# Kernel tuning notes

Measured on AMD Instinct MI355X. Metric: run time of the kernel, lower is better.

The kernel has to match this reference:

```python
import jax, jax.numpy as jnp
import numpy as np


def setup_inputs() -> dict:
    key = jax.random.key(0)
    k1, k2 = jax.random.split(key)
    B, S, V = 4, 2048, 32000
    y_pred = jax.random.normal(k1, (B, S, V), dtype=jnp.float32)
    y_true = jax.random.randint(k2, (B, S), 0, V, dtype=jnp.int64)
    return {"y_pred": y_pred, "y_true": y_true, "pad_id": 0}


def reference(y_pred, y_true, pad_id):
    # Shift: predict token t+1 from position t (per the torch loop's [:-1]/[1:]).
    logits = y_pred[:, :-1, :]        # (B, S-1, V)
    targets = y_true[:, 1:]           # (B, S-1)
    logp = jax.nn.log_softmax(logits, axis=-1)
    # Gather log-prob of the true token: fused log-softmax + gather.
    nll = -jnp.take_along_axis(logp, targets[..., None], axis=-1)[..., 0]  # (B, S-1)
    mask = (targets != pad_id).astype(logits.dtype)
    # Per-sequence mean over non-pad tokens, then mean over batch.
    per_seq = jnp.sum(nll * mask, axis=-1) / jnp.sum(mask, axis=-1)        # (B,)
    return jnp.mean(per_seq)
```

## Files before the change

kernel.cpp:

```cpp
#include <hip/hip_runtime.h>
#include <math.h>

#define VOCAB 32000
#define SEQ   2048
#define SM1   2047
#define BATCH 4

__global__ __launch_bounds__(256)
void ce_row_kernel(const float* __restrict__ y_pred,
                   const int*   __restrict__ y_true,
                   const int*   __restrict__ pad_id_p,
                   float* __restrict__ row_nll,
                   float* __restrict__ row_msk) {
    const int row = blockIdx.x;
    const int b   = row / SM1;
    const int s   = row % SM1;
    const int tid = threadIdx.x;

    const float*  rowp  = y_pred + ((size_t)b * SEQ + s) * (size_t)VOCAB;
    const float4* rowp4 = (const float4*)rowp;

    float m    = -INFINITY;
    float ssum = 0.0f;
    for (int i = tid; i < VOCAB / 4; i += 256) {
        float4 v  = rowp4[i];
        float  m4 = fmaxf(fmaxf(v.x, v.y), fmaxf(v.z, v.w));
        if (m4 > m) {
            ssum *= __expf(m - m4);
            m = m4;
        }
        ssum += __expf(v.x - m) + __expf(v.y - m)
              + __expf(v.z - m) + __expf(v.w - m);
    }

    __shared__ float sm_m[256];
    __shared__ float sm_s[256];
    sm_m[tid] = m;
    sm_s[tid] = ssum;
    __syncthreads();
    for (int off = 128; off > 0; off >>= 1) {
        if (tid < off) {
            float m1 = sm_m[tid],       s1 = sm_s[tid];
            float m2 = sm_m[tid + off], s2 = sm_s[tid + off];
            float mm = fmaxf(m1, m2);
            sm_m[tid] = mm;
            sm_s[tid] = s1 * __expf(m1 - mm) + s2 * __expf(m2 - mm);
        }
        __syncthreads();
    }

    if (tid == 0) {
        const int tgt = y_true[b * SEQ + s + 1];
        const int pad = pad_id_p[0];
        const float xt  = rowp[tgt];
        const float nll = logf(sm_s[0]) + sm_m[0] - xt;
        const float mk  = (tgt != pad) ? 1.0f : 0.0f;
        row_nll[row] = nll * mk;
        row_msk[row] = mk;
    }
}

__global__ __launch_bounds__(256)
void ce_final_kernel(const float* __restrict__ row_nll,
                     const float* __restrict__ row_msk,
                     float* __restrict__ out) {
    __shared__ float sm[256];
    const int tid = threadIdx.x;
    float acc = 0.0f;
    for (int b = 0; b < BATCH; ++b) {
        float sn = 0.0f, sc = 0.0f;
        for (int i = tid; i < SM1; i += 256) {
            sn += row_nll[b * SM1 + i];
            sc += row_msk[b * SM1 + i];
        }
        sm[tid] = sn; __syncthreads();
        for (int off = 128; off > 0; off >>= 1) {
            if (tid < off) sm[tid] += sm[tid + off];
            __syncthreads();
        }
        float tot_n = sm[0];
        __syncthreads();
        sm[tid] = sc; __syncthreads();
        for (int off = 128; off > 0; off >>= 1) {
            if (tid < off) sm[tid] += sm[tid + off];
            __syncthreads();
        }
        float tot_c = sm[0];
        __syncthreads();
        acc += tot_n / tot_c;
    }
    if (tid == 0) out[0] = acc / (float)BATCH;
}

extern "C" void kernel_launch(void* const* d_in, const int* in_sizes, int n_in,
                              void* d_out, int out_size, void* d_ws, size_t ws_size,
                              hipStream_t stream) {
    const float* y_pred = (const float*)d_in[0];
    const int*   y_true = (const int*)d_in[1];
    const int*   pad_id = (const int*)d_in[2];
    float* out = (float*)d_out;

    float* row_nll = (float*)d_ws;
    float* row_msk = row_nll + BATCH * SM1;

    ce_row_kernel<<<BATCH * SM1, 256, 0, stream>>>(y_pred, y_true, pad_id,
                                                   row_nll, row_msk);
    ce_final_kernel<<<1, 256, 0, stream>>>(row_nll, row_msk, out);
}
```

Before: 198.6 us.

## Use 320-thread exact-trip loop, nontemporal loads, and wave-shuffle online-softmax reduction

The row kernel now runs 320 threads so the 8000 float4 chunks divide exactly into 25 iterations, unrolled by 5. Loads use nontemporal hints, the sum is split into four independent accumulators, and the block reduction uses wave-level xor shuffles followed by a tiny serial combine of the five wave partials. Together these aim to cut LDS traffic and barriers, raise memory-level parallelism and add streaming cache hints on a purely bandwidth-bound pass. The trade-offs are slightly higher register pressure and a non-power-of-two block size.

```diff
diff --git a/kernel.cpp b/kernel.cpp
--- a/kernel.cpp
+++ b/kernel.cpp
@@ -5,8 +5,11 @@
 #define SEQ   2048
 #define SM1   2047
 #define BATCH 4
+#define NTHR  320
 
-__global__ __launch_bounds__(256)
+typedef float floatx4 __attribute__((ext_vector_type(4)));
+
+__global__ __launch_bounds__(NTHR)
 void ce_row_kernel(const float* __restrict__ y_pred,
                    const int*   __restrict__ y_true,
                    const int*   __restrict__ pad_id_p,
@@ -17,43 +20,56 @@
     const int s   = row % SM1;
     const int tid = threadIdx.x;
 
-    const float*  rowp  = y_pred + ((size_t)b * SEQ + s) * (size_t)VOCAB;
-    const float4* rowp4 = (const float4*)rowp;
+    const float*   rowp  = y_pred + ((size_t)b * SEQ + s) * (size_t)VOCAB;
+    const floatx4* rowp4 = (const floatx4*)rowp;
 
-    float m    = -INFINITY;
-    float ssum = 0.0f;
-    for (int i = tid; i < VOCAB / 4; i += 256) {
-        float4 v  = rowp4[i];
-        float  m4 = fmaxf(fmaxf(v.x, v.y), fmaxf(v.z, v.w));
+    float m  = -INFINITY;
+    float p0 = 0.0f, p1 = 0.0f, p2 = 0.0f, p3 = 0.0f;
+
+#pragma unroll 5
+    for (int it = 0; it < 25; ++it) {
+        const int i = tid + it * NTHR;
+        floatx4 v = __builtin_nontemporal_load(&rowp4[i]);
+        float m4 = fmaxf(fmaxf(v.x, v.y), fmaxf(v.z, v.w));
         if (m4 > m) {
-            ssum *= __expf(m - m4);
+            const float r = __expf(m - m4);
+            p0 *= r; p1 *= r; p2 *= r; p3 *= r;
             m = m4;
         }
-        ssum += __expf(v.x - m) + __expf(v.y - m)
-              + __expf(v.z - m) + __expf(v.w - m);
+        p0 += __expf(v.x - m);
+        p1 += __expf(v.y - m);
+        p2 += __expf(v.z - m);
+        p3 += __expf(v.w - m);
+    }
+    float ssum = (p0 + p1) + (p2 + p3);
+
+    for (int off = 32; off > 0; off >>= 1) {
+        const float m2 = __shfl_xor(m, off);
+        const float s2 = __shfl_xor(ssum, off);
+        const float mm = fmaxf(m, m2);
+        ssum = ssum * __expf(m - mm) + s2 * __expf(m2 - mm);
+        m = mm;
     }
 
-    __shared__ float sm_m[256];
-    __shared__ float sm_s[256];
-    sm_m[tid] = m;
-    sm_s[tid] = ssum;
+    __shared__ float sm_m[NTHR / 64];
+    __shared__ float sm_s[NTHR / 64];
+    const int wid = tid >> 6;
+    if ((tid & 63) == 0) { sm_m[wid] = m; sm_s[wid] = ssum; }
     __syncthreads();
-    for (int off = 128; off > 0; off >>= 1) {
-        if (tid < off) {
-            float m1 = sm_m[tid],       s1 = sm_s[tid];
-            float m2 = sm_m[tid + off], s2 = sm_s[tid + off];
-            float mm = fmaxf(m1, m2);
-            sm_m[tid] = mm;
-            sm_s[tid] = s1 * __expf(m1 - mm) + s2 * __expf(m2 - mm);
-        }
-        __syncthreads();
-    }
 
     if (tid == 0) {
+        float M = sm_m[0], S = sm_s[0];
+#pragma unroll
+        for (int w = 1; w < NTHR / 64; ++w) {
+            const float m2 = sm_m[w], s2 = sm_s[w];
+            const float mm = fmaxf(M, m2);
+            S = S * __expf(M - mm) + s2 * __expf(m2 - mm);
+            M = mm;
+        }
         const int tgt = y_true[b * SEQ + s + 1];
         const int pad = pad_id_p[0];
         const float xt  = rowp[tgt];
-        const float nll = logf(sm_s[0]) + sm_m[0] - xt;
+        const float nll = logf(S) + M - xt;
         const float mk  = (tgt != pad) ? 1.0f : 0.0f;
         row_nll[row] = nll * mk;
         row_msk[row] = mk;
@@ -78,14 +94,14 @@
             if (tid < off) sm[tid] += sm[tid + off];
             __syncthreads();
         }
-        float tot_n = sm[0];
+        const float tot_n = sm[0];
         __syncthreads();
         sm[tid] = sc; __syncthreads();
         for (int off = 128; off > 0; off >>= 1) {
             if (tid < off) sm[tid] += sm[tid + off];
             __syncthreads();
         }
-        float tot_c = sm[0];
+        const float tot_c = sm[0];
         __syncthreads();
         acc += tot_n / tot_c;
     }
@@ -103,7 +119,7 @@
     float* row_nll = (float*)d_ws;
     float* row_msk = row_nll + BATCH * SM1;
 
-    ce_row_kernel<<<BATCH * SM1, 256, 0, stream>>>(y_pred, y_true, pad_id,
-                                                   row_nll, row_msk);
+    ce_row_kernel<<<BATCH * SM1, NTHR, 0, stream>>>(y_pred, y_true, pad_id,
+                                                    row_nll, row_msk);
     ce_final_kernel<<<1, 256, 0, stream>>>(row_nll, row_msk, out);
 }
```

Result: faster. 170.4 us (-14.2%).
